# Optimization experiments

Measured on AMD Instinct MI355X. Metric: run time of the kernel, lower is better.

Reference implementation:

```python
import jax, jax.numpy as jnp
import numpy as np

HEADS = 4
HEAD_DIM = 128  # GATConv out_channels
NEG_SLOPE_ATT = 0.2   # GATConv internal leaky relu
NEG_SLOPE_ACT = 0.01  # nn.LeakyReLU() default


def gat_conv(x, edge_index, W, att_src, att_dst, bias):
    # x: [N, F]; edge_index: [2, E] (row 0 = src j, row 1 = dst i)
    N = x.shape[0]
    h = (x @ W).reshape(N, HEADS, HEAD_DIM)            # [N, H, C]
    loops = jnp.arange(N, dtype=edge_index.dtype)
    src = jnp.concatenate([edge_index[0], loops])      # add self loops
    dst = jnp.concatenate([edge_index[1], loops])
    a_src = jnp.einsum('nhc,hc->nh', h, att_src)       # [N, H]
    a_dst = jnp.einsum('nhc,hc->nh', h, att_dst)
    e = jax.nn.leaky_relu(a_src[src] + a_dst[dst], NEG_SLOPE_ATT)  # [E', H]
    # segment softmax over incoming edges of each dst node
    emax = jax.ops.segment_max(e, dst, num_segments=N)
    ex = jnp.exp(e - emax[dst])
    denom = jax.ops.segment_sum(ex, dst, num_segments=N)
    alpha = ex / (denom[dst] + 1e-16)                  # [E', H]
    msg = h[src] * alpha[:, :, None]                   # [E', H, C]
    out = jax.ops.segment_sum(msg, dst, num_segments=N)
    return out.reshape(N, HEADS * HEAD_DIM) + bias     # [N, H*C]


def branch(x, edge_index, W, att_src, att_dst, bias, fc1_w, fc1_b):
    h = gat_conv(x, edge_index, W, att_src, att_dst, bias)
    h = jax.nn.leaky_relu(h, NEG_SLOPE_ACT)
    g = jnp.mean(h, axis=0, keepdims=True)             # global mean pool, batch all zeros -> [1, H*C]
    g = jax.nn.leaky_relu(g @ fc1_w + fc1_b, NEG_SLOPE_ACT)
    return g  # dropout is identity in eval mode


def setup_inputs() -> dict:
    key = jax.random.key(0)
    ks = jax.random.split(key, 10)
    N, E, F = 20000, 320000, 512
    HC = HEADS * HEAD_DIM
    s = 1.0 / np.sqrt(F)
    return {
        'x': jax.random.normal(ks[0], (N, F), jnp.float32),
        'adj': jax.random.randint(ks[1], (2, E), 0, N, jnp.int64),
        'wt_x': jax.random.normal(ks[2], (N, F), jnp.float32),
        'wt_adj': jax.random.randint(ks[3], (2, E), 0, N, jnp.int64),
        'W': jax.random.normal(ks[4], (F, HC), jnp.float32) * s,
        'att_src': jax.random.normal(ks[5], (HEADS, HEAD_DIM), jnp.float32) * s,
        'att_dst': jax.random.normal(ks[6], (HEADS, HEAD_DIM), jnp.float32) * s,
        'bias': jnp.zeros((HC,), jnp.float32),
        'fc1_w': jax.random.normal(ks[7], (HC, 512), jnp.float32) * (1.0 / np.sqrt(HC)),
        'fc1_b': jnp.zeros((512,), jnp.float32),
    }


def reference(x, adj, wt_x, wt_adj, W, att_src, att_dst, bias, fc1_w, fc1_b):
    g = branch(x, adj, W, att_src, att_dst, bias, fc1_w, fc1_b)
    wt_g = branch(wt_x, wt_adj, W, att_src, att_dst, bias, fc1_w, fc1_b)
    xd = g - wt_g
    return jnp.concatenate([g, wt_g, xd], axis=1)  # [1, 3*512]
```

## Files before the change

kernel.cpp:

```cpp
#include <hip/hip_runtime.h>
#include <hip/hip_bf16.h>

typedef unsigned short u16;
typedef short bf16x8 __attribute__((ext_vector_type(8)));
typedef float f32x4 __attribute__((ext_vector_type(4)));
typedef float f32x2 __attribute__((ext_vector_type(2)));

__device__ __forceinline__ u16 f2b(float f) {
    unsigned x = __float_as_uint(f);
    return (u16)((x + 0x7fffu + ((x >> 16) & 1u)) >> 16);
}

__device__ __forceinline__ int pkbf(float lo, float hi) {
    return __builtin_amdgcn_perm(__float_as_uint(hi), __float_as_uint(lo), 0x07060302);
}

__device__ __forceinline__ void pkfma(f32x2& acc, f32x2 f, f32x2 ex) {
    asm("v_pk_fma_f32 %0, %1, %2, %0" : "+v"(acc) : "v"(f), "v"(ex));
}

__global__ void cast_wt_kernel(const float* __restrict__ W, u16* __restrict__ Wt) {
    int idx = blockIdx.x * blockDim.x + threadIdx.x;
    int n = idx >> 9, k = idx & 511;
    Wt[idx] = f2b(W[k * 512 + n]);
}

__global__ __launch_bounds__(256, 2) void gemm_fused2(
    const float* __restrict__ xA, const float* __restrict__ xW, const u16* __restrict__ Bt,
    unsigned char* __restrict__ h8, const float* __restrict__ att_src,
    const float* __restrict__ att_dst, float* __restrict__ asrc, float* __restrict__ adst,
    int N, int Mpad) {
    __shared__ float lA[128 * 32];
    __shared__ u16 lB[128 * 32];
    __shared__ float sred[2][128][2];
    const int tid = threadIdx.x;
    const int w = tid >> 6, l = tid & 63;
    const int row0 = blockIdx.y * 128;
    const int head = blockIdx.x;
    const int col0 = head * 128;
    const int wr = w >> 1, wc = w & 1;
    const int mlane = l & 15, quad = l >> 4;
    const int R2v = 2 * Mpad;

    const float* src = (row0 >= Mpad) ? xW : xA;
    const int rbase = row0 - (row0 >= Mpad ? Mpad : 0);
    const int arow = (w << 3) + (l >> 3);
    const int acol = (l & 7) << 2;
    const int srow = (w << 4) + (l >> 2);
    const int scol = (l & 3) << 3;

    f32x4 acc[4][4];
#pragma unroll
    for (int i = 0; i < 4; i++)
#pragma unroll
        for (int j = 0; j < 4; j++) acc[i][j] = f32x4{0.f, 0.f, 0.f, 0.f};

    for (int k0 = 0; k0 < 512; k0 += 32) {
#pragma unroll
        for (int g = 0; g < 4; ++g) {
            int lrow = rbase + g * 32 + arow;
            lrow = min(lrow, N - 1);
            const float* ga = src + (size_t)lrow * 512 + k0 + acol;
            float* la = lA + (g * 32 + (w << 3)) * 32;
            __builtin_amdgcn_global_load_lds((const __attribute__((address_space(1))) void*)ga,
                                             (__attribute__((address_space(3))) void*)la, 16, 0, 0);
        }
#pragma unroll
        for (int s = 0; s < 2; ++s) {
            const u16* gb = Bt + (size_t)(col0 + s * 64 + srow) * 512 + (k0 + scol);
            u16* lb = lB + s * 2048 + w * 512;
            __builtin_amdgcn_global_load_lds((const __attribute__((address_space(1))) void*)gb,
                                             (__attribute__((address_space(3))) void*)lb, 16, 0, 0);
        }
        __syncthreads();
        bf16x8 af[4], bfr[4];
#pragma unroll
        for (int i = 0; i < 4; i++) {
            const float* ap = &lA[(wr * 64 + i * 16 + mlane) * 32 + quad * 8];
            float4 f0 = *(const float4*)ap;
            float4 f1 = *(const float4*)(ap + 4);
            int* ai = (int*)&af[i];
            ai[0] = pkbf(f0.x, f0.y);
            ai[1] = pkbf(f0.z, f0.w);
            ai[2] = pkbf(f1.x, f1.y);
            ai[3] = pkbf(f1.z, f1.w);
            bfr[i] = *(const bf16x8*)&lB[(wc * 64 + i * 16 + mlane) * 32 + quad * 8];
        }
#pragma unroll
        for (int i = 0; i < 4; i++)
#pragma unroll
            for (int j = 0; j < 4; j++)
                acc[i][j] = __builtin_amdgcn_mfma_f32_16x16x32_bf16(af[i], bfr[j], acc[i][j], 0, 0, 0);
        __syncthreads();
    }

    float as_j[4], ad_j[4];
#pragma unroll
    for (int j = 0; j < 4; j++) {
        as_j[j] = att_src[col0 + wc * 64 + j * 16 + mlane];
        ad_j[j] = att_dst[col0 + wc * 64 + j * 16 + mlane];
    }
#pragma unroll
    for (int i = 0; i < 4; i++) {
#pragma unroll
        for (int r = 0; r < 4; r++) {
            float vs = 0.f, vd = 0.f;
#pragma unroll
            for (int j = 0; j < 4; j++) {
                float hv = acc[i][j][r];
                vs += hv * as_j[j];
                vd += hv * ad_j[j];
            }
#pragma unroll
            for (int o = 8; o >= 1; o >>= 1) {
                vs += __shfl_xor(vs, o);
                vd += __shfl_xor(vd, o);
            }
            if (mlane == 0) {
                int lrow = wr * 64 + i * 16 + quad * 4 + r;
                sred[0][lrow][wc] = vs;
                sred[1][lrow][wc] = vd;
            }
        }
    }
#pragma unroll
    for (int i = 0; i < 4; i++)
#pragma unroll
        for (int j = 0; j < 4; j++)
#pragma unroll
            for (int r = 0; r < 4; r++) {
                int rg = row0 + wr * 64 + i * 16 + quad * 4 + r;
                int cc = wc * 64 + j * 16 + mlane;
                float v = acc[i][j][r];
                unsigned pk = __builtin_amdgcn_cvt_pk_fp8_f32(v, v, 0, false);
                h8[(((size_t)(head * R2v + rg)) << 7) + cc] = (unsigned char)(pk & 0xff);
            }
    __syncthreads();
    {
        int row = tid & 127, which = tid >> 7;
        int rg = row0 + row;
        float v = sred[which][row][0] + sred[which][row][1];
        (which ? adst : asrc)[head * R2v + rg] = v;
    }
}

__global__ void csr_count(const int* __restrict__ adj, const int* __restrict__ wadj,
                          int E, int Mpad, int* __restrict__ deg) {
    int i = blockIdx.x * blockDim.x + threadIdx.x;
    if (i < 2 * E) {
        int d = (i < E) ? adj[E + i] : (wadj[E + (i - E)] + Mpad);
        atomicAdd(&deg[d], 1);
    }
}

__global__ __launch_bounds__(256) void scanA(const int* __restrict__ deg, int* __restrict__ off,
                                             int* __restrict__ bsum, int n, int N, int Mpad) {
    __shared__ int wsum[4];
    int tid = threadIdx.x, lane = tid & 63, wid = tid >> 6;
    int i = blockIdx.x * 256 + tid;
    int valid = (i < N) || (i >= Mpad && i < Mpad + N);
    int d = (i < n) ? deg[i] + (valid ? 1 : 0) : 0;
    int x = d;
#pragma unroll
    for (int o = 1; o < 64; o <<= 1) {
        int y = __shfl_up(x, (unsigned)o, 64);
        if (lane >= o) x += y;
    }
    if (lane == 63) wsum[wid] = x;
    __syncthreads();
    int woff = 0;
    for (int j = 0; j < wid; ++j) woff += wsum[j];
    if (i < n) off[i] = woff + x - d;
    if (tid == 255) bsum[blockIdx.x] = woff + x;
}

__global__ __launch_bounds__(256) void scanB(const int* __restrict__ bsum, int* __restrict__ bbase,
                                             int nb, int* __restrict__ off, int n) {
    __shared__ int wsum[4];
    int tid = threadIdx.x, lane = tid & 63, wid = tid >> 6;
    int d = (tid < nb) ? bsum[tid] : 0;
    int x = d;
#pragma unroll
    for (int o = 1; o < 64; o <<= 1) {
        int y = __shfl_up(x, (unsigned)o, 64);
        if (lane >= o) x += y;
    }
    if (lane == 63) wsum[wid] = x;
    __syncthreads();
    int woff = 0;
    for (int j = 0; j < wid; ++j) woff += wsum[j];
    int excl = woff + x - d;
    if (tid < nb) bbase[tid] = excl;
    if (tid == nb - 1) off[n] = excl + d;
}

__global__ void scanC(int* __restrict__ off, const int* __restrict__ bbase,
                      int* __restrict__ cursor, int* __restrict__ csrc, int n, int N, int Mpad) {
    int i = blockIdx.x * blockDim.x + threadIdx.x;
    if (i < n) {
        int o = off[i] + bbase[i >> 8];
        off[i] = o;
        int valid = (i < N) || (i >= Mpad && i < Mpad + N);
        if (valid) csrc[o] = i;
        cursor[i] = o + valid;
    }
}

__global__ void csr_scatter(const int* __restrict__ adj, const int* __restrict__ wadj,
                            int E, int Mpad, int* __restrict__ cursor, int* __restrict__ csrc) {
    int i = blockIdx.x * blockDim.x + threadIdx.x;
    if (i < 2 * E) {
        int s, d;
        if (i < E) {
            s = adj[i];
            d = adj[E + i];
        } else {
            s = wadj[i - E] + Mpad;
            d = wadj[E + (i - E)] + Mpad;
        }
        int p = atomicAdd(&cursor[d], 1);
        csrc[p] = s;
    }
}

__global__ __launch_bounds__(256) void gat_aggregate9(
    const unsigned char* __restrict__ h8, const float* __restrict__ asrc,
    const float* __restrict__ adst, const int* __restrict__ off, const int* __restrict__ csrc,
    const float* __restrict__ bias, float* __restrict__ partAB, int Mpad, int Em1) {
    const int R2 = 2 * Mpad;
    __shared__ float spool[256];
    int tid = threadIdx.x;
    spool[tid] = 0.f;
    __syncthreads();
    const int wv = tid >> 6, l = tid & 63;
    const int gi = (l >> 3) & 3;
    const int hi = l >> 5;
    const int chb = (l & 7) << 4;
    const int head = (blockIdx.x & 7) >> 1;
    const unsigned char* h8h = h8 + (((size_t)head * R2) << 7);
    const float* ash = asrc + (size_t)head * R2;
    const float* adh = adst + (size_t)head * R2;
    float bb[16];
#pragma unroll
    for (int k = 0; k < 16; ++k) bb[k] = bias[head * 128 + chb + k];
    float pool[16];
#pragma unroll
    for (int k = 0; k < 16; ++k) pool[k] = 0.f;

    int widx = ((((blockIdx.x >> 3) << 1) | (blockIdx.x & 1)) << 2) + wv;
    int hf = widx >> 10;
    int aw = widx & 1023;
    const int hb = hf * Mpad;
    const int half = Mpad >> 1;

    for (int p = aw; p < half; p += 1024) {
        int d0 = (p << 1) + hb;
        int q0 = off[d0], q1 = off[d0 + 1], q2 = off[d0 + 2];
        int n0 = q1 - q0, n1 = q2 - q1;
        int nmax = max(n0, n1);
        if (nmax == 0) continue;
        int nm = hi ? n1 : n0;
        int qm = hi ? q1 : q0;
        float ad = adh[d0 + hi];
        f32x2 acc2[8];
#pragma unroll
        for (int j = 0; j < 8; ++j) acc2[j] = f32x2{0.f, 0.f};
        float dsum = 0.f;

        int i0 = gi;
        int e0 = csrc[min(qm + ((i0 < nm) ? i0 : 0), Em1)];
        float acur = ash[e0];
        int4 hcur = *(const int4*)(h8h + (((size_t)e0) << 7) + chb);
        int i1 = 4 + gi;
        int enext = csrc[min(qm + ((i1 < nm) ? i1 : 0), Em1)];

        for (int base = 0; base < nmax; base += 4) {
            float anext = ash[enext];
            int4 hnext = *(const int4*)(h8h + (((size_t)enext) << 7) + chb);
            int i2 = base + 8 + gi;
            int e2 = csrc[min(qm + ((i2 < nm) ? i2 : 0), Em1)];
            float e = acur + ad;
            float em = fmaxf(e, 0.2f * e);
            float ex = __expf(em);
            ex = ((base + gi) < nm) ? ex : 0.f;
            dsum += ex;
            f32x2 exv = {ex, ex};
            f32x2 f;
            f = __builtin_amdgcn_cvt_pk_f32_fp8(hcur.x, false); pkfma(acc2[0], f, exv);
            f = __builtin_amdgcn_cvt_pk_f32_fp8(hcur.x, true);  pkfma(acc2[1], f, exv);
            f = __builtin_amdgcn_cvt_pk_f32_fp8(hcur.y, false); pkfma(acc2[2], f, exv);
            f = __builtin_amdgcn_cvt_pk_f32_fp8(hcur.y, true);  pkfma(acc2[3], f, exv);
            f = __builtin_amdgcn_cvt_pk_f32_fp8(hcur.z, false); pkfma(acc2[4], f, exv);
            f = __builtin_amdgcn_cvt_pk_f32_fp8(hcur.z, true);  pkfma(acc2[5], f, exv);
            f = __builtin_amdgcn_cvt_pk_f32_fp8(hcur.w, false); pkfma(acc2[6], f, exv);
            f = __builtin_amdgcn_cvt_pk_f32_fp8(hcur.w, true);  pkfma(acc2[7], f, exv);
            acur = anext; hcur = hnext; enext = e2;
        }
        dsum += __shfl_xor(dsum, 8);
        dsum += __shfl_xor(dsum, 16);
#pragma unroll
        for (int j = 0; j < 8; ++j) {
            acc2[j].x += __shfl_xor(acc2[j].x, 8);
            acc2[j].y += __shfl_xor(acc2[j].y, 8);
            acc2[j].x += __shfl_xor(acc2[j].x, 16);
            acc2[j].y += __shfl_xor(acc2[j].y, 16);
        }
        if (nm > 0) {
            float inv = 1.f / (dsum + 1e-16f);
#pragma unroll
            for (int j = 0; j < 8; ++j) {
                float o0 = acc2[j].x * inv + bb[2 * j];
                float o1 = acc2[j].y * inv + bb[2 * j + 1];
                pool[2 * j] += fmaxf(o0, 0.01f * o0);
                pool[2 * j + 1] += fmaxf(o1, 0.01f * o1);
            }
        }
    }
    if ((l & 31) < 8) {
#pragma unroll
        for (int k = 0; k < 16; ++k) atomicAdd(&spool[hf * 128 + chb + k], pool[k]);
    }
    __syncthreads();
    {
        int base = (blockIdx.x & 63) << 9;
        int c = tid & 127;
        float v = spool[tid];
        float* dp = (tid < 128) ? (partAB + base + head * 128 + c)
                                : (partAB + 64 * 512 + base + head * 128 + c);
        atomicAdd(dp, v);
    }
}

__global__ __launch_bounds__(256) void fc_final2(
    const float* __restrict__ partAB, const float* __restrict__ w, const float* __restrict__ b,
    float* __restrict__ out, float invN) {
    __shared__ float gA[512], gB[512];
    __shared__ float rA[256], rB[256];
    int t = threadIdx.x;
    for (int i = t; i < 512; i += 256) {
        float sA = 0.f, sB = 0.f;
        for (int r = 0; r < 64; ++r) {
            sA += partAB[r * 512 + i];
            sB += partAB[64 * 512 + r * 512 + i];
        }
        gA[i] = sA * invN;
        gB[i] = sB * invN;
    }
    __syncthreads();
    int jj = t & 31, ks = t >> 5;
    int j = blockIdx.x * 32 + jj;
    float sA = 0.f, sB = 0.f;
    for (int k = ks * 64; k < ks * 64 + 64; ++k) {
        float wv = w[k * 512 + j];
        sA += gA[k] * wv;
        sB += gB[k] * wv;
    }
    rA[t] = sA;
    rB[t] = sB;
    __syncthreads();
    if (ks == 0) {
#pragma unroll
        for (int s2 = 1; s2 < 8; ++s2) {
            sA += rA[jj + 32 * s2];
            sB += rB[jj + 32 * s2];
        }
        sA += b[j];
        sB += b[j];
        sA = sA >= 0.f ? sA : 0.01f * sA;
        sB = sB >= 0.f ? sB : 0.01f * sB;
        out[j] = sA;
        out[512 + j] = sB;
        out[1024 + j] = sA - sB;
    }
}

extern "C" void kernel_launch(void* const* d_in, const int* in_sizes, int n_in,
                              void* d_out, int out_size, void* d_ws, size_t ws_size,
                              hipStream_t stream) {
    const float* x = (const float*)d_in[0];
    const int* adj = (const int*)d_in[1];
    const float* wtx = (const float*)d_in[2];
    const int* wadj = (const int*)d_in[3];
    const float* W = (const float*)d_in[4];
    const float* att_s = (const float*)d_in[5];
    const float* att_d = (const float*)d_in[6];
    const float* bias = (const float*)d_in[7];
    const float* fc1w = (const float*)d_in[8];
    const float* fc1b = (const float*)d_in[9];
    float* out = (float*)d_out;

    const int N = in_sizes[0] / 512;
    const int E = in_sizes[1] / 2;
    const int Mpad = ((N + 127) / 128) * 128;
    const int R2 = 2 * Mpad;
    const int nb = (R2 + 255) / 256;

    char* p = (char*)d_ws;
    auto alloc = [&](size_t bytes) -> char* {
        char* r = p;
        p += (bytes + 255) & ~(size_t)255;
        return r;
    };
    unsigned char* h8 = (unsigned char*)alloc((size_t)R2 * 512);
    u16* Wt = (u16*)alloc(512 * 512 * 2);
    float* asrc = (float*)alloc((size_t)R2 * 4 * 4);
    float* adst = (float*)alloc((size_t)R2 * 4 * 4);
    int* deg = (int*)alloc((size_t)R2 * 4);
    int* off = (int*)alloc((size_t)(R2 + 1) * 4);
    int* cursor = (int*)alloc((size_t)R2 * 4);
    int* bsum = (int*)alloc(256 * 4);
    int* bbase = (int*)alloc(256 * 4);
    int* csrc = (int*)alloc((size_t)2 * (E + N) * 4);
    float* partAB = (float*)alloc((size_t)2 * 64 * 512 * 4);

    hipMemsetAsync(partAB, 0, (size_t)2 * 64 * 512 * 4, stream);
    hipMemsetAsync(deg, 0, (size_t)R2 * 4, stream);
    cast_wt_kernel<<<(512 * 512) / 256, 256, 0, stream>>>(W, Wt);

    csr_count<<<(2 * E + 255) / 256, 256, 0, stream>>>(adj, wadj, E, Mpad, deg);
    scanA<<<nb, 256, 0, stream>>>(deg, off, bsum, R2, N, Mpad);
    scanB<<<1, 256, 0, stream>>>(bsum, bbase, nb, off, R2);
    scanC<<<nb, 256, 0, stream>>>(off, bbase, cursor, csrc, R2, N, Mpad);
    csr_scatter<<<(2 * E + 255) / 256, 256, 0, stream>>>(adj, wadj, E, Mpad, cursor, csrc);

    dim3 gg(4, R2 / 128, 1);
    gemm_fused2<<<gg, 256, 0, stream>>>(x, wtx, Wt, h8, att_s, att_d, asrc, adst, N, Mpad);

    gat_aggregate9<<<2048, 256, 0, stream>>>(h8, asrc, adst, off, csrc, bias, partAB, Mpad,
                                             2 * (E + N) - 1);

    fc_final2<<<16, 256, 0, stream>>>(partAB, fc1w, fc1b, out, 1.0f / (float)N);
}
```

Before: 349.0 us.

## Deepen gather prefetch pipeline and remap blocks to a single graph

The GAT aggregation loop now keeps two gathered feature rows and four source indices in flight instead of one, to hide more of the latency of the random h8/asrc gathers. Each block is also tied to one graph (gc from blockIdx bit 0), which halves the shared pool and the final atomics, and the index clamp to Em1 is dropped. Launch bounds request 8 waves per SIMD. The deeper pipeline raises register pressure. Removing the clamp relies on the padded csrc reads staying inside the allocation.

```diff
diff --git a/kernel.cpp b/kernel.cpp
--- a/kernel.cpp
+++ b/kernel.cpp
@@ -223,20 +223,21 @@
     }
 }
 
-__global__ __launch_bounds__(256) void gat_aggregate9(
+__global__ __launch_bounds__(256, 8) void gat_aggregate10(
     const unsigned char* __restrict__ h8, const float* __restrict__ asrc,
     const float* __restrict__ adst, const int* __restrict__ off, const int* __restrict__ csrc,
-    const float* __restrict__ bias, float* __restrict__ partAB, int Mpad, int Em1) {
+    const float* __restrict__ bias, float* __restrict__ partAB, int Mpad) {
     const int R2 = 2 * Mpad;
-    __shared__ float spool[256];
+    __shared__ float spool[128];
     int tid = threadIdx.x;
-    spool[tid] = 0.f;
+    if (tid < 128) spool[tid] = 0.f;
     __syncthreads();
     const int wv = tid >> 6, l = tid & 63;
     const int gi = (l >> 3) & 3;
     const int hi = l >> 5;
     const int chb = (l & 7) << 4;
     const int head = (blockIdx.x & 7) >> 1;
+    const int gc = blockIdx.x & 1;
     const unsigned char* h8h = h8 + (((size_t)head * R2) << 7);
     const float* ash = asrc + (size_t)head * R2;
     const float* adh = adst + (size_t)head * R2;
@@ -247,13 +248,11 @@
 #pragma unroll
     for (int k = 0; k < 16; ++k) pool[k] = 0.f;
 
-    int widx = ((((blockIdx.x >> 3) << 1) | (blockIdx.x & 1)) << 2) + wv;
-    int hf = widx >> 10;
-    int aw = widx & 1023;
-    const int hb = hf * Mpad;
+    const int hb = gc * Mpad;
     const int half = Mpad >> 1;
-
-    for (int p = aw; p < half; p += 1024) {
+    int widx = ((blockIdx.x >> 3) << 2) + wv;
+
+    for (int p = widx; p < half; p += 1024) {
         int d0 = (p << 1) + hb;
         int q0 = off[d0], q1 = off[d0 + 1], q2 = off[d0 + 2];
         int n0 = q1 - q0, n1 = q2 - q1;
@@ -267,34 +266,39 @@
         for (int j = 0; j < 8; ++j) acc2[j] = f32x2{0.f, 0.f};
         float dsum = 0.f;
 
-        int i0 = gi;
-        int e0 = csrc[min(qm + ((i0 < nm) ? i0 : 0), Em1)];
-        float acur = ash[e0];
-        int4 hcur = *(const int4*)(h8h + (((size_t)e0) << 7) + chb);
-        int i1 = 4 + gi;
-        int enext = csrc[min(qm + ((i1 < nm) ? i1 : 0), Em1)];
+        int i0 = gi, i1 = 4 + gi, i2 = 8 + gi, i3 = 12 + gi;
+        int E0 = csrc[qm + ((i0 < nm) ? i0 : 0)];
+        int E1 = csrc[qm + ((i1 < nm) ? i1 : 0)];
+        int E2 = csrc[qm + ((i2 < nm) ? i2 : 0)];
+        int E3 = csrc[qm + ((i3 < nm) ? i3 : 0)];
+        float A0 = ash[E0];
+        int4 H0 = *(const int4*)(h8h + (((size_t)E0) << 7) + chb);
+        float A1 = ash[E1];
+        int4 H1 = *(const int4*)(h8h + (((size_t)E1) << 7) + chb);
 
         for (int base = 0; base < nmax; base += 4) {
-            float anext = ash[enext];
-            int4 hnext = *(const int4*)(h8h + (((size_t)enext) << 7) + chb);
-            int i2 = base + 8 + gi;
-            int e2 = csrc[min(qm + ((i2 < nm) ? i2 : 0), Em1)];
-            float e = acur + ad;
+            int i4 = base + 16 + gi;
+            int E4 = csrc[qm + ((i4 < nm) ? i4 : 0)];
+            float A2 = ash[E2];
+            int4 H2 = *(const int4*)(h8h + (((size_t)E2) << 7) + chb);
+            float e = A0 + ad;
             float em = fmaxf(e, 0.2f * e);
             float ex = __expf(em);
             ex = ((base + gi) < nm) ? ex : 0.f;
             dsum += ex;
             f32x2 exv = {ex, ex};
             f32x2 f;
-            f = __builtin_amdgcn_cvt_pk_f32_fp8(hcur.x, false); pkfma(acc2[0], f, exv);
-            f = __builtin_amdgcn_cvt_pk_f32_fp8(hcur.x, true);  pkfma(acc2[1], f, exv);
-            f = __builtin_amdgcn_cvt_pk_f32_fp8(hcur.y, false); pkfma(acc2[2], f, exv);
-            f = __builtin_amdgcn_cvt_pk_f32_fp8(hcur.y, true);  pkfma(acc2[3], f, exv);
-            f = __builtin_amdgcn_cvt_pk_f32_fp8(hcur.z, false); pkfma(acc2[4], f, exv);
-            f = __builtin_amdgcn_cvt_pk_f32_fp8(hcur.z, true);  pkfma(acc2[5], f, exv);
-            f = __builtin_amdgcn_cvt_pk_f32_fp8(hcur.w, false); pkfma(acc2[6], f, exv);
-            f = __builtin_amdgcn_cvt_pk_f32_fp8(hcur.w, true);  pkfma(acc2[7], f, exv);
-            acur = anext; hcur = hnext; enext = e2;
+            f = __builtin_amdgcn_cvt_pk_f32_fp8(H0.x, false); pkfma(acc2[0], f, exv);
+            f = __builtin_amdgcn_cvt_pk_f32_fp8(H0.x, true);  pkfma(acc2[1], f, exv);
+            f = __builtin_amdgcn_cvt_pk_f32_fp8(H0.y, false); pkfma(acc2[2], f, exv);
+            f = __builtin_amdgcn_cvt_pk_f32_fp8(H0.y, true);  pkfma(acc2[3], f, exv);
+            f = __builtin_amdgcn_cvt_pk_f32_fp8(H0.z, false); pkfma(acc2[4], f, exv);
+            f = __builtin_amdgcn_cvt_pk_f32_fp8(H0.z, true);  pkfma(acc2[5], f, exv);
+            f = __builtin_amdgcn_cvt_pk_f32_fp8(H0.w, false); pkfma(acc2[6], f, exv);
+            f = __builtin_amdgcn_cvt_pk_f32_fp8(H0.w, true);  pkfma(acc2[7], f, exv);
+            A0 = A1; H0 = H1;
+            A1 = A2; H1 = H2;
+            E2 = E3; E3 = E4;
         }
         dsum += __shfl_xor(dsum, 8);
         dsum += __shfl_xor(dsum, 16);
@@ -318,16 +322,13 @@
     }
     if ((l & 31) < 8) {
 #pragma unroll
-        for (int k = 0; k < 16; ++k) atomicAdd(&spool[hf * 128 + chb + k], pool[k]);
-    }
-    __syncthreads();
-    {
-        int base = (blockIdx.x & 63) << 9;
-        int c = tid & 127;
-        float v = spool[tid];
-        float* dp = (tid < 128) ? (partAB + base + head * 128 + c)
-                                : (partAB + 64 * 512 + base + head * 128 + c);
-        atomicAdd(dp, v);
+        for (int k = 0; k < 16; ++k) atomicAdd(&spool[chb + k], pool[k]);
+    }
+    __syncthreads();
+    if (tid < 128) {
+        int slot = (blockIdx.x >> 3) & 63;
+        float* dp = partAB + (gc ? 64 * 512 : 0) + (slot << 9) + head * 128 + tid;
+        atomicAdd(dp, spool[tid]);
     }
 }
 
@@ -426,8 +427,7 @@
     dim3 gg(4, R2 / 128, 1);
     gemm_fused2<<<gg, 256, 0, stream>>>(x, wtx, Wt, h8, att_s, att_d, asrc, adst, N, Mpad);
 
-    gat_aggregate9<<<2048, 256, 0, stream>>>(h8, asrc, adst, off, csrc, bias, partAB, Mpad,
-                                             2 * (E + N) - 1);
+    gat_aggregate10<<<2048, 256, 0, stream>>>(h8, asrc, adst, off, csrc, bias, partAB, Mpad);
 
     fc_final2<<<16, 256, 0, stream>>>(partAB, fc1w, fc1b, out, 1.0f / (float)N);
 }
```

Result: slower. 357.0 us (+2.3%).
